# Optimization experiments

Hardware: AMD Instinct MI355X
Metric: run time of the kernel (lower is better)

Reference implementation:

```python
import jax, jax.numpy as jnp
import numpy as np

CHUNK = 256  # points per lax.map step; keeps [CHUNK, F] intermediates small


def _point_tri_sqdist(p_chunk, a, b, c):
    """Squared distance from each point to each triangle (Ericson closest-point).
    p_chunk: [C,3]; a,b,c: [F,3] -> returns [C,F]."""
    p = p_chunk[:, None, :]          # [C,1,3]
    a = a[None]; b = b[None]; c = c[None]  # [1,F,3]
    ab = b - a
    ac = c - a
    ap = p - a
    d1 = jnp.sum(ab * ap, -1)
    d2 = jnp.sum(ac * ap, -1)
    bp = p - b
    d3 = jnp.sum(ab * bp, -1)
    d4 = jnp.sum(ac * bp, -1)
    cp = p - c
    d5 = jnp.sum(ab * cp, -1)
    d6 = jnp.sum(ac * cp, -1)
    vc_ = d1 * d4 - d3 * d2
    vb_ = d5 * d2 - d1 * d6
    va_ = d3 * d6 - d5 * d4
    # safe-guarded edge / interior parameters
    den_ab = d1 - d3
    v_ab = d1 / jnp.where(den_ab != 0, den_ab, 1.0)
    den_ac = d2 - d6
    w_ac = d2 / jnp.where(den_ac != 0, den_ac, 1.0)
    den_bc = (d4 - d3) + (d5 - d6)
    w_bc = (d4 - d3) / jnp.where(den_bc != 0, den_bc, 1.0)
    den_in = va_ + vb_ + vc_
    inv = 1.0 / jnp.where(den_in != 0, den_in, 1.0)
    v_in = vb_ * inv
    w_in = vc_ * inv
    # candidate closest point; later writes take priority (vertex regions last)
    q = a + ab * v_in[..., None] + ac * w_in[..., None]                      # interior
    q = jnp.where(((va_ <= 0) & (d4 - d3 >= 0) & (d5 - d6 >= 0))[..., None],
                  b + (c - b) * w_bc[..., None], q)                          # edge bc
    q = jnp.where(((vb_ <= 0) & (d2 >= 0) & (d6 <= 0))[..., None],
                  a + ac * w_ac[..., None], q)                               # edge ac
    q = jnp.where(((vc_ <= 0) & (d1 >= 0) & (d3 <= 0))[..., None],
                  a + ab * v_ab[..., None], q)                               # edge ab
    q = jnp.where(((d6 >= 0) & (d5 <= d6))[..., None], c, q)                 # vertex c
    q = jnp.where(((d3 >= 0) & (d4 <= d3))[..., None], b, q)                 # vertex b
    q = jnp.where(((d1 <= 0) & (d2 <= 0))[..., None], a, q)                  # vertex a
    return jnp.sum((p - q) ** 2, -1)


def _mesh_sdf(verts, faces, points):
    va = verts[faces[:, 0]]
    vb = verts[faces[:, 1]]
    vc = verts[faces[:, 2]]

    def per_chunk(pc):
        d = _point_tri_sqdist(pc, va, vb, vc)   # [CHUNK, F]
        return jnp.min(d, axis=-1), jnp.argmin(d, axis=-1)

    P = points.shape[0]
    dists, assoc = jax.lax.map(per_chunk, points.reshape(P // CHUNK, CHUNK, 3))
    dist = dists.reshape(P)
    assoc = assoc.reshape(P).astype(jnp.int32)
    loss = jnp.sum(dist)
    return loss, dist, assoc


def setup_inputs() -> dict:
    key = jax.random.key(0)
    k1, k2, k3 = jax.random.split(key, 3)
    V, F, P = 8192, 16384, 16384
    verts = jax.random.uniform(k1, (V, 3), dtype=jnp.float32)
    faces = jax.random.randint(k2, (F, 3), 0, V, dtype=jnp.int32)
    points = jax.random.uniform(k3, (P, 3), dtype=jnp.float32)
    return {"verts": verts, "faces": faces, "points": points}


def reference(verts, faces, points):
    return _mesh_sdf(verts, faces, points)
```

## Files before the change

### kernel.cpp

```cpp
#include <hip/hip_runtime.h>
#include <math.h>


#define PTOT 16384
#define FTOT 16384
#define NBINS 4096
#define BLOCK 256
#define NCH 16
#define FCHUNK (FTOT / NCH)
#define TILE 256
#define QD 16

#define WS_BEST    0
#define WS_SORTP   131072
#define WS_HISTP   393216
#define WS_HISTF   409600
#define WS_HISTFC  425984
#define WS_FA      442368
#define WS_FB      704512
#define WS_FC      966656
#define WS_FSPH    1228800
#define WS_FSCAN   1490944
#define WS_FK      1753088

__device__ __forceinline__ unsigned morton12(float x, float y, float z) {
    int ix = (int)(x * 16.0f); ix = ix < 0 ? 0 : (ix > 15 ? 15 : ix);
    int iy = (int)(y * 16.0f); iy = iy < 0 ? 0 : (iy > 15 ? 15 : iy);
    int iz = (int)(z * 16.0f); iz = iz < 0 ? 0 : (iz > 15 ? 15 : iz);
    unsigned code = 0;
#pragma unroll
    for (int k = 0; k < 4; ++k) {
        code |= (((unsigned)(ix >> k) & 1u) << (3 * k + 2))
              | (((unsigned)(iy >> k) & 1u) << (3 * k + 1))
              | (((unsigned)(iz >> k) & 1u) << (3 * k + 0));
    }
    return code;
}

__device__ __forceinline__ float exec_pair(
    float px, float py, float pz,
    float ax, float ay, float az,
    float bx, float by, float bz,
    float cx, float cy, float cz)
{
#pragma clang fp contract(off)
    const float abx = __fsub_rn(bx, ax), aby = __fsub_rn(by, ay), abz = __fsub_rn(bz, az);
    const float acx = __fsub_rn(cx, ax), acy = __fsub_rn(cy, ay), acz = __fsub_rn(cz, az);
    const float cbx = __fsub_rn(cx, bx), cby = __fsub_rn(cy, by), cbz = __fsub_rn(cz, bz);

    const float apx = __fsub_rn(px, ax), apy = __fsub_rn(py, ay), apz = __fsub_rn(pz, az);
    const float d1 = __fadd_rn(__fadd_rn(__fmul_rn(abx, apx), __fmul_rn(aby, apy)), __fmul_rn(abz, apz));
    const float d2 = __fadd_rn(__fadd_rn(__fmul_rn(acx, apx), __fmul_rn(acy, apy)), __fmul_rn(acz, apz));
    const float bpx = __fsub_rn(px, bx), bpy = __fsub_rn(py, by), bpz = __fsub_rn(pz, bz);
    const float d3 = __fadd_rn(__fadd_rn(__fmul_rn(abx, bpx), __fmul_rn(aby, bpy)), __fmul_rn(abz, bpz));
    const float d4 = __fadd_rn(__fadd_rn(__fmul_rn(acx, bpx), __fmul_rn(acy, bpy)), __fmul_rn(acz, bpz));
    const float cpx = __fsub_rn(px, cx), cpy = __fsub_rn(py, cy), cpz = __fsub_rn(pz, cz);
    const float d5 = __fadd_rn(__fadd_rn(__fmul_rn(abx, cpx), __fmul_rn(aby, cpy)), __fmul_rn(abz, cpz));
    const float d6 = __fadd_rn(__fadd_rn(__fmul_rn(acx, cpx), __fmul_rn(acy, cpy)), __fmul_rn(acz, cpz));

    const float vc_ = __fsub_rn(__fmul_rn(d1, d4), __fmul_rn(d3, d2));
    const float vb_ = __fsub_rn(__fmul_rn(d5, d2), __fmul_rn(d1, d6));
    const float va_ = __fsub_rn(__fmul_rn(d3, d6), __fmul_rn(d5, d4));

    const float den_ab = __fsub_rn(d1, d3);
    const float den_ac = __fsub_rn(d2, d6);
    const float t43    = __fsub_rn(d4, d3);
    const float t56    = __fsub_rn(d5, d6);
    const float den_bc = __fadd_rn(t43, t56);
    const float den_in = __fadd_rn(__fadd_rn(va_, vb_), vc_);

    const bool f_a  = (d1 <= 0.0f) && (d2 <= 0.0f);
    const bool f_b  = (d3 >= 0.0f) && (d4 <= d3);
    const bool f_c  = (d6 >= 0.0f) && (d5 <= d6);
    const bool f_ab = (vc_ <= 0.0f) && (d1 >= 0.0f) && (d3 <= 0.0f);
    const bool f_ac = (vb_ <= 0.0f) && (d2 >= 0.0f) && (d6 <= 0.0f);
    const bool f_bc = (va_ <= 0.0f) && (t43 >= 0.0f) && (t56 >= 0.0f);
    const bool vert = f_a || f_b || f_c;
    const bool e_ab = f_ab && !vert;
    const bool e_ac = f_ac && !vert && !f_ab;
    const bool e_bc = f_bc && !vert && !f_ab && !f_ac;
    const bool inte = !vert && !f_ab && !f_ac && !f_bc;

    const float num  = e_ab ? d1 : (e_ac ? d2 : (e_bc ? t43 : 1.0f));
    const float denr = e_ab ? den_ab : (e_ac ? den_ac : (e_bc ? den_bc : den_in));
    const float den  = (denr != 0.0f) ? denr : 1.0f;
    const float t    = __fdiv_rn(num, den);

    const float v_in = __fmul_rn(vb_, t);
    const float w_in = __fmul_rn(vc_, t);

    const float s1 = vert ? 0.0f : (inte ? v_in : t);
    const float s2 = inte ? w_in : 0.0f;
    const bool  sel_b = (!f_a && f_b) || e_bc;
    const bool  sel_c = !f_a && !f_b && f_c;
    const float e1x = e_ac ? acx : (e_bc ? cbx : abx);
    const float e1y = e_ac ? acy : (e_bc ? cby : aby);
    const float e1z = e_ac ? acz : (e_bc ? cbz : abz);
    const float bsx = sel_b ? bx : (sel_c ? cx : ax);
    const float bsy = sel_b ? by : (sel_c ? cy : ay);
    const float bsz = sel_b ? bz : (sel_c ? cz : az);
    const float qx = __fadd_rn(__fadd_rn(bsx, __fmul_rn(e1x, s1)), __fmul_rn(acx, s2));
    const float qy = __fadd_rn(__fadd_rn(bsy, __fmul_rn(e1y, s1)), __fmul_rn(acy, s2));
    const float qz = __fadd_rn(__fadd_rn(bsz, __fmul_rn(e1z, s1)), __fmul_rn(acz, s2));

    const float dxx = __fsub_rn(px, qx), dyy = __fsub_rn(py, qy), dzz = __fsub_rn(pz, qz);
    return __fadd_rn(__fadd_rn(__fmul_rn(dxx, dxx), __fmul_rn(dyy, dyy)), __fmul_rn(dzz, dzz));
}

__global__ __launch_bounds__(BLOCK) void hist_kernel(
    const float* __restrict__ verts, const int* __restrict__ faces,
    const float* __restrict__ points,
    unsigned* __restrict__ histP, unsigned* __restrict__ histF)
{
    const int b = blockIdx.x;
    if (b < 64) {
        const int p = b * BLOCK + threadIdx.x;
        atomicAdd(&histP[morton12(points[p*3], points[p*3+1], points[p*3+2])], 1u);
    } else {
        const int f = (b - 64) * BLOCK + threadIdx.x;
        const int i0 = faces[f*3+0], i1 = faces[f*3+1], i2 = faces[f*3+2];
        const float mx = (verts[i0*3+0] + verts[i1*3+0] + verts[i2*3+0]) * (1.0f/3.0f);
        const float my = (verts[i0*3+1] + verts[i1*3+1] + verts[i2*3+1]) * (1.0f/3.0f);
        const float mz = (verts[i0*3+2] + verts[i1*3+2] + verts[i2*3+2]) * (1.0f/3.0f);
        atomicAdd(&histF[morton12(mx, my, mz)], 1u);
    }
}

__global__ __launch_bounds__(256) void scan_kernel(
    unsigned* __restrict__ histP, unsigned* __restrict__ histF,
    unsigned* __restrict__ histFC)
{
    unsigned* h = (blockIdx.x == 0) ? histP : histF;
    __shared__ unsigned ps[256];
    const int t = threadIdx.x;
    unsigned local[16];
    unsigned run = 0;
#pragma unroll
    for (int i = 0; i < 16; ++i) { unsigned v = h[t*16+i]; local[i] = run; run += v; }
    ps[t] = run;
    __syncthreads();
    for (int off = 1; off < 256; off <<= 1) {
        unsigned v = (t >= off) ? ps[t - off] : 0u;
        __syncthreads();
        ps[t] += v;
        __syncthreads();
    }
    const unsigned base = (t == 0) ? 0u : ps[t-1];
#pragma unroll
    for (int i = 0; i < 16; ++i) {
        const unsigned off = base + local[i];
        h[t*16+i] = off;
        if (blockIdx.x == 1) histFC[t*16+i] = off;
    }
}

__global__ __launch_bounds__(BLOCK) void scatter_build_kernel(
    const float* __restrict__ verts, const int* __restrict__ faces,
    const float* __restrict__ points,
    unsigned* __restrict__ histP, unsigned* __restrict__ histF,
    uint4* __restrict__ sortP,
    float4* __restrict__ fA, float4* __restrict__ fB, float4* __restrict__ fC,
    float4* __restrict__ fSph, float4* __restrict__ fScan,
    float2* __restrict__ fK)
{
    const int b = blockIdx.x;
    if (b < 64) {
        const int p = b * BLOCK + threadIdx.x;
        const float x = points[p*3], y = points[p*3+1], z = points[p*3+2];
        const unsigned pos = atomicAdd(&histP[morton12(x, y, z)], 1u);
        sortP[pos] = make_uint4(__float_as_uint(x), __float_as_uint(y),
                                __float_as_uint(z), (unsigned)p);
        return;
    }
    const int f = (b - 64) * BLOCK + threadIdx.x;
    const int i0 = faces[f*3+0], i1 = faces[f*3+1], i2 = faces[f*3+2];
    const float ax = verts[i0*3+0], ay = verts[i0*3+1], az = verts[i0*3+2];
    const float bx = verts[i1*3+0], by = verts[i1*3+1], bz = verts[i1*3+2];
    const float cx = verts[i2*3+0], cy = verts[i2*3+1], cz = verts[i2*3+2];
    const float mx = (ax+bx+cx) * (1.0f/3.0f);
    const float my = (ay+by+cy) * (1.0f/3.0f);
    const float mz = (az+bz+cz) * (1.0f/3.0f);
    const unsigned pos = atomicAdd(&histF[morton12(mx, my, mz)], 1u);

    fA[pos] = make_float4(ax, ay, az, __uint_as_float((unsigned)f));
    fB[pos] = make_float4(bx, by, bz, 0.0f);
    fC[pos] = make_float4(cx, cy, cz, 0.0f);

    const double abx = (double)bx-ax, aby = (double)by-ay, abz = (double)bz-az;
    const double acx = (double)cx-ax, acy = (double)cy-ay, acz = (double)cz-az;
    const double cbx = (double)cx-bx, cby = (double)cy-by, cbz = (double)cz-bz;
    const double nx = aby*acz - abz*acy;
    const double ny = abz*acx - abx*acz;
    const double nz = abx*acy - aby*acx;
    const double nn = nx*nx + ny*ny + nz*nz;
    const double e1 = sqrt(abx*abx + aby*aby + abz*abz);
    const double e2 = sqrt(acx*acx + acy*acy + acz*acz);
    const double e3 = sqrt(cbx*cbx + cby*cby + cbz*cbz);
    const double maxe = fmax(e1, fmax(e2, e3));
    const double mine = fmin(e1, fmin(e2, e3));
    const double mine2 = mine * mine;
    const double maxe2 = maxe * maxe;
    const double maxe3 = maxe2 * maxe;

    const bool exempt = !(nn > 1e-5 * maxe2) || !(mine2 > 5e-6 * maxe);

    float4 sc;
    float kp, J;
    if (!exempt) {
        const double rin = 1.0 / sqrt(nn);
        sc.x = (float)(nx * rin);
        sc.y = (float)(ny * rin);
        sc.z = (float)(nz * rin);
        sc.w = (float)(-(nx*rin*ax + ny*rin*ay + nz*rin*az));
        kp = (float)fmin(1e4, 3e-5 * maxe3 / nn + 2e-5);
        J  = (float)fmin(1e4, 1.2 * (6e-5 * maxe3 / nn
                                   + 5e-5 * maxe2 / mine2
                                   + 2.6e-6 * maxe / mine
                                   + 3.2e-3));
    } else {
        sc = make_float4(0.0f, 0.0f, 0.0f, 0.0f);
        kp = 1e4f;
        J  = 1e30f;
    }
    fScan[pos] = sc;
    fK[pos] = make_float2(kp, J);

    const double ra = sqrt(((double)ax-mx)*((double)ax-mx) + ((double)ay-my)*((double)ay-my) + ((double)az-mz)*((double)az-mz));
    const double rb = sqrt(((double)bx-mx)*((double)bx-mx) + ((double)by-my)*((double)by-my) + ((double)bz-mz)*((double)bz-mz));
    const double rc = sqrt(((double)cx-mx)*((double)cx-mx) + ((double)cy-my)*((double)cy-my) + ((double)cz-mz)*((double)cz-mz));
    const float rf = (float)(fmax(ra, fmax(rb, rc)) * 1.0002 + 2e-4);
    fSph[pos] = make_float4(mx, my, mz, rf);
}

__global__ __launch_bounds__(BLOCK) void sdf_main_kernel(
    const uint4* __restrict__ sortP,
    const unsigned* __restrict__ histFC,
    const float4* __restrict__ fA, const float4* __restrict__ fB,
    const float4* __restrict__ fC, const float4* __restrict__ fSph,
    const float4* __restrict__ fScan, const float2* __restrict__ fK,
    unsigned long long* __restrict__ best)
{
    __shared__ float4 sScan[TILE], sSph[TILE], sA[TILE], sB[TILE], sC[TILE];
    __shared__ float2 sK[TILE];
    __shared__ unsigned short sQ[TILE * QD];

    const int tid = threadIdx.x;
    const uint4 sp = sortP[blockIdx.x * BLOCK + tid];
    const float px = __uint_as_float(sp.x);
    const float py = __uint_as_float(sp.y);
    const float pz = __uint_as_float(sp.z);
    const int  pid = (int)sp.w;

    unsigned long long bestPk = ~0ull;
    {
        const unsigned code = morton12(px, py, pz);
        int w = (int)histFC[code] - 16;
        w = w < 0 ? 0 : (w > FTOT - 32 ? FTOT - 32 : w);
#pragma unroll
        for (int s = 0; s < 2; ++s) {
            const int i = w + 2 * (int)blockIdx.y + s;
            const float4 A = fA[i], B = fB[i], C = fC[i];
            const float d = exec_pair(px, py, pz, A.x, A.y, A.z, B.x, B.y, B.z, C.x, C.y, C.z);
            const unsigned long long pk =
                ((unsigned long long)__float_as_uint(d) << 32) | __float_as_uint(A.w);
            if (pk < bestPk) bestPk = pk;
        }
    }
    {
        const unsigned long long old = atomicMin(&best[pid], bestPk);
        if (old < bestPk) bestPk = old;
    }
    float pruneS = sqrtf(__uint_as_float((unsigned)(bestPk >> 32)));
    float thr    = __fmaf_rn(pruneS, 1.005f, 1e-3f);

    const int fbase = (int)blockIdx.y * FCHUNK;
    int cnt = 0;

    auto drain = [&]() {
        for (int k = 0; ; ++k) {
            if (!__ballot(k < cnt)) break;
            if (k < cnt) {
                const int j = (int)sQ[tid * QD + k];
                const float4 sc = sScan[j];
                const float4 S  = sSph[j];
                const float dx = px - S.x, dy = py - S.y, dz = pz - S.z;
                const float dcc2 = __fmaf_rn(dx, dx, __fmaf_rn(dy, dy, dz * dz));
                const float pdc  = __fmaf_rn(sc.x, dx, __fmaf_rn(sc.y, dy, sc.z * dz));
                const float pd   = __fmaf_rn(sc.x, px, __fmaf_rn(sc.y, py, __fmaf_rn(sc.z, pz, sc.w)));
                const float aa   = fmaxf(fabsf(pd) - 1e-5f, 0.0f);
                const float lat2 = fmaxf(dcc2 - pdc * pdc, 0.0f);
                const float lat  = fmaxf(sqrtf(lat2) * 0.999f - S.w - 1e-4f, 0.0f);
                const float lhs  = __fmaf_rn(aa, aa, lat * lat);
                const float rhs  = thr + sK[j].y;
                if (!(lhs > rhs * rhs)) {
                    const float4 A = sA[j], B = sB[j], C = sC[j];
                    const float d = exec_pair(px, py, pz, A.x, A.y, A.z, B.x, B.y, B.z, C.x, C.y, C.z);
                    const unsigned long long pk =
                        ((unsigned long long)__float_as_uint(d) << 32) | __float_as_uint(A.w);
                    if (pk < bestPk) {
                        bestPk = pk;
                        pruneS = fminf(pruneS, sqrtf(d));
                        thr    = __fmaf_rn(pruneS, 1.005f, 1e-3f);
                    }
                }
            }
        }
        cnt = 0;
    };

    for (int t0 = 0; t0 < FCHUNK; t0 += TILE) {
        __syncthreads();
        {
            const int g = fbase + t0 + tid;
            sScan[tid] = fScan[g];
            sSph[tid]  = fSph[g];
            sK[tid]    = fK[g];
            sA[tid]    = fA[g];
            sB[tid]    = fB[g];
            sC[tid]    = fC[g];
        }
        __syncthreads();

        {
            const unsigned long long gb =
                __hip_atomic_load(&best[pid], __ATOMIC_RELAXED, __HIP_MEMORY_SCOPE_AGENT);
            if (gb < bestPk) bestPk = gb;
            pruneS = fminf(pruneS, sqrtf(__uint_as_float((unsigned)(bestPk >> 32))));
            thr    = __fmaf_rn(pruneS, 1.005f, 1e-3f);
        }

        for (int j0 = 0; j0 < TILE; j0 += 8) {
#pragma unroll
            for (int j = j0; j < j0 + 8; ++j) {
                const float4 sc = sScan[j];
                const float pd = __fmaf_rn(sc.x, px, __fmaf_rn(sc.y, py, __fmaf_rn(sc.z, pz, sc.w)));
                const bool inband = !(fabsf(pd) > (thr + sK[j].x));
                if (inband) { sQ[tid * QD + cnt] = (unsigned short)j; ++cnt; }
            }
            if (__any(cnt >= QD - 8)) drain();
        }
        drain();
    }

    atomicMin(&best[pid], bestPk);
}

__global__ __launch_bounds__(BLOCK) void sdf_final_kernel(
    const unsigned long long* __restrict__ best, float* __restrict__ out)
{
    __shared__ float wsum[BLOCK / 64];
    const int p = blockIdx.x * BLOCK + threadIdx.x;
    const unsigned long long v = best[p];
    const float d = __uint_as_float((unsigned)(v >> 32));
    const int idx = (int)(unsigned)(v & 0xffffffffull);
    out[1 + p] = d;
    out[1 + PTOT + p] = (float)idx;

    float s = d;
    for (int off = 32; off > 0; off >>= 1) s += __shfl_down(s, off, 64);
    const int lane = threadIdx.x & 63;
    const int w = threadIdx.x >> 6;
    if (lane == 0) wsum[w] = s;
    __syncthreads();
    if (threadIdx.x == 0) {
        float tsum = 0.0f;
        for (int i = 0; i < BLOCK / 64; ++i) tsum += wsum[i];
        atomicAdd(&out[0], tsum);
    }
}

extern "C" void kernel_launch(void* const* d_in, const int* in_sizes, int n_in,
                              void* d_out, int out_size, void* d_ws, size_t ws_size,
                              hipStream_t stream) {
    const float* verts  = (const float*)d_in[0];
    const int*   faces  = (const int*)d_in[1];
    const float* points = (const float*)d_in[2];
    float* out = (float*)d_out;

    char* ws = (char*)d_ws;
    unsigned long long* best = (unsigned long long*)(ws + WS_BEST);
    uint4*    sortP  = (uint4*)(ws + WS_SORTP);
    unsigned* histP  = (unsigned*)(ws + WS_HISTP);
    unsigned* histF  = (unsigned*)(ws + WS_HISTF);
    unsigned* histFC = (unsigned*)(ws + WS_HISTFC);
    float4* fA    = (float4*)(ws + WS_FA);
    float4* fB    = (float4*)(ws + WS_FB);
    float4* fC    = (float4*)(ws + WS_FC);
    float4* fSph  = (float4*)(ws + WS_FSPH);
    float4* fScan = (float4*)(ws + WS_FSCAN);
    float2* fK    = (float2*)(ws + WS_FK);

    hipMemsetAsync(best, 0xFF, (size_t)PTOT * sizeof(unsigned long long), stream);
    hipMemsetAsync(histP, 0, 2 * (size_t)NBINS * sizeof(unsigned), stream);
    hipMemsetAsync(out, 0, sizeof(float), stream);

    hist_kernel<<<128, BLOCK, 0, stream>>>(verts, faces, points, histP, histF);
    scan_kernel<<<2, 256, 0, stream>>>(histP, histF, histFC);
    scatter_build_kernel<<<128, BLOCK, 0, stream>>>(verts, faces, points,
        histP, histF, sortP, fA, fB, fC, fSph, fScan, fK);

    dim3 grid(PTOT / BLOCK, NCH);
    sdf_main_kernel<<<grid, BLOCK, 0, stream>>>(sortP, histFC,
        fA, fB, fC, fSph, fScan, fK, best);
    sdf_final_kernel<<<PTOT / BLOCK, BLOCK, 0, stream>>>(best, out);
}
```

Measured before the change: 371.2 us.

## Double face-chunk split and read triangle vertices from global memory

Raises the number of face chunks per point block from 16 to 32, so the grid has twice as many blocks, each scanning half as many faces. Triangle vertex arrays are no longer staged in LDS. The exact distance test now reads A/B/C from global memory (L2/L1) only for faces that survive pruning, and the initial seed evaluates one nearby face instead of two. The intent is more parallelism and less LDS traffic and footprint, at the cost of more atomics, more redundant tile loads of the scan data, and scattered global reads. The old drain lambda is left behind as dead code.

```diff
diff --git a/kernel.cpp b/kernel.cpp
--- a/kernel.cpp
+++ b/kernel.cpp
@@ -6,7 +6,7 @@
 #define FTOT 16384
 #define NBINS 4096
 #define BLOCK 256
-#define NCH 16
+#define NCH 32
 #define FCHUNK (FTOT / NCH)
 #define TILE 256
 #define QD 16
@@ -240,7 +240,8 @@
     const float4* __restrict__ fScan, const float2* __restrict__ fK,
     unsigned long long* __restrict__ best)
 {
-    __shared__ float4 sScan[TILE], sSph[TILE], sA[TILE], sB[TILE], sC[TILE];
+    __shared__ float4 sScan[TILE];
+    __shared__ float4 sSph[TILE];
     __shared__ float2 sK[TILE];
     __shared__ unsigned short sQ[TILE * QD];
 
@@ -256,15 +257,10 @@
         const unsigned code = morton12(px, py, pz);
         int w = (int)histFC[code] - 16;
         w = w < 0 ? 0 : (w > FTOT - 32 ? FTOT - 32 : w);
-#pragma unroll
-        for (int s = 0; s < 2; ++s) {
-            const int i = w + 2 * (int)blockIdx.y + s;
-            const float4 A = fA[i], B = fB[i], C = fC[i];
-            const float d = exec_pair(px, py, pz, A.x, A.y, A.z, B.x, B.y, B.z, C.x, C.y, C.z);
-            const unsigned long long pk =
-                ((unsigned long long)__float_as_uint(d) << 32) | __float_as_uint(A.w);
-            if (pk < bestPk) bestPk = pk;
-        }
+        const int i = w + (int)blockIdx.y;
+        const float4 A = fA[i], B = fB[i], C = fC[i];
+        const float d = exec_pair(px, py, pz, A.x, A.y, A.z, B.x, B.y, B.z, C.x, C.y, C.z);
+        bestPk = ((unsigned long long)__float_as_uint(d) << 32) | __float_as_uint(A.w);
     }
     {
         const unsigned long long old = atomicMin(&best[pid], bestPk);
@@ -293,31 +289,25 @@
                 const float lhs  = __fmaf_rn(aa, aa, lat * lat);
                 const float rhs  = thr + sK[j].y;
                 if (!(lhs > rhs * rhs)) {
-                    const float4 A = sA[j], B = sB[j], C = sC[j];
-                    const float d = exec_pair(px, py, pz, A.x, A.y, A.z, B.x, B.y, B.z, C.x, C.y, C.z);
-                    const unsigned long long pk =
-                        ((unsigned long long)__float_as_uint(d) << 32) | __float_as_uint(A.w);
-                    if (pk < bestPk) {
-                        bestPk = pk;
-                        pruneS = fminf(pruneS, sqrtf(d));
-                        thr    = __fmaf_rn(pruneS, 1.005f, 1e-3f);
-                    }
+                    const int gi = fbase  + j;
+                    (void)gi;
+                    const int fi = (int)sQ[tid * QD + k] + 0;
+                    (void)fi;
                 }
             }
         }
         cnt = 0;
     };
+    (void)drain;
 
     for (int t0 = 0; t0 < FCHUNK; t0 += TILE) {
+        const int tileBase = fbase + t0;
         __syncthreads();
         {
-            const int g = fbase + t0 + tid;
+            const int g = tileBase + tid;
             sScan[tid] = fScan[g];
             sSph[tid]  = fSph[g];
             sK[tid]    = fK[g];
-            sA[tid]    = fA[g];
-            sB[tid]    = fB[g];
-            sC[tid]    = fC[g];
         }
         __syncthreads();
 
@@ -328,6 +318,40 @@
             pruneS = fminf(pruneS, sqrtf(__uint_as_float((unsigned)(bestPk >> 32))));
             thr    = __fmaf_rn(pruneS, 1.005f, 1e-3f);
         }
+
+        auto drainT = [&]() {
+            for (int k = 0; ; ++k) {
+                if (!__ballot(k < cnt)) break;
+                if (k < cnt) {
+                    const int j = (int)sQ[tid * QD + k];
+                    const float4 sc = sScan[j];
+                    const float4 S  = sSph[j];
+                    const float dx = px - S.x, dy = py - S.y, dz = pz - S.z;
+                    const float dcc2 = __fmaf_rn(dx, dx, __fmaf_rn(dy, dy, dz * dz));
+                    const float pdc  = __fmaf_rn(sc.x, dx, __fmaf_rn(sc.y, dy, sc.z * dz));
+                    const float pd   = __fmaf_rn(sc.x, px, __fmaf_rn(sc.y, py, __fmaf_rn(sc.z, pz, sc.w)));
+                    const float aa   = fmaxf(fabsf(pd) - 1e-5f, 0.0f);
+                    const float lat2 = fmaxf(dcc2 - pdc * pdc, 0.0f);
+                    const float lat  = fmaxf(sqrtf(lat2) * 0.999f - S.w - 1e-4f, 0.0f);
+                    const float lhs  = __fmaf_rn(aa, aa, lat * lat);
+                    const float rhs  = thr + sK[j].y;
+                    if (!(lhs > rhs * rhs)) {
+                        const int fi = tileBase + j;
+                        const float4 A = fA[fi], B = fB[fi], C = fC[fi];
+                        const float d = exec_pair(px, py, pz,
+                            A.x, A.y, A.z, B.x, B.y, B.z, C.x, C.y, C.z);
+                        const unsigned long long pk =
+                            ((unsigned long long)__float_as_uint(d) << 32) | __float_as_uint(A.w);
+                        if (pk < bestPk) {
+                            bestPk = pk;
+                            pruneS = fminf(pruneS, sqrtf(d));
+                            thr    = __fmaf_rn(pruneS, 1.005f, 1e-3f);
+                        }
+                    }
+                }
+            }
+            cnt = 0;
+        };
 
         for (int j0 = 0; j0 < TILE; j0 += 8) {
 #pragma unroll
@@ -337,9 +361,9 @@
                 const bool inband = !(fabsf(pd) > (thr + sK[j].x));
                 if (inband) { sQ[tid * QD + cnt] = (unsigned short)j; ++cnt; }
             }
-            if (__any(cnt >= QD - 8)) drain();
+            if (__any(cnt >= QD - 8)) drainT();
         }
-        drain();
+        drainT();
     }
 
     atomicMin(&best[pid], bestPk);
```

Result: no change. 366.7 us (-1.2%).

## Drop sphere/J secondary culling, use per-tile max slab width, split faces into 32 chunks

Applied to the files above, without the earlier changes.

The per-face bounding-sphere and J-bound secondary test is removed, and the per-face slab width is replaced by a per-256-face tile maximum built with atomicMax. Candidate triangle vertices are now read from global memory instead of shared memory, and shared usage drops to the plane array and the queue. The face dimension is split across 32 chunks instead of 16, the queue write becomes branchless with a transposed layout, and the best distance is published after each tile. This trades fewer shared loads and higher occupancy for weaker pruning, so more exact point-triangle evaluations run, and it adds a coarser tile-level bound.

```diff
diff --git a/kernel.cpp b/kernel.cpp
--- a/kernel.cpp
+++ b/kernel.cpp
@@ -6,7 +6,7 @@
 #define FTOT 16384
 #define NBINS 4096
 #define BLOCK 256
-#define NCH 16
+#define NCH 32
 #define FCHUNK (FTOT / NCH)
 #define TILE 256
 #define QD 16
@@ -15,13 +15,13 @@
 #define WS_SORTP   131072
 #define WS_HISTP   393216
 #define WS_HISTF   409600
-#define WS_HISTFC  425984
-#define WS_FA      442368
-#define WS_FB      704512
-#define WS_FC      966656
-#define WS_FSPH    1228800
-#define WS_FSCAN   1490944
-#define WS_FK      1753088
+#define WS_TILEKP  425984
+#define WS_HISTFC  426240
+#define WS_FA      442624
+#define WS_FB      704768
+#define WS_FC      966912
+#define WS_FSCAN   1229056
+#define ZERO_BYTES (16384 + 16384 + 256)
 
 __device__ __forceinline__ unsigned morton12(float x, float y, float z) {
     int ix = (int)(x * 16.0f); ix = ix < 0 ? 0 : (ix > 15 ? 15 : ix);
@@ -160,8 +160,7 @@
     unsigned* __restrict__ histP, unsigned* __restrict__ histF,
     uint4* __restrict__ sortP,
     float4* __restrict__ fA, float4* __restrict__ fB, float4* __restrict__ fC,
-    float4* __restrict__ fSph, float4* __restrict__ fScan,
-    float2* __restrict__ fK)
+    float4* __restrict__ fScan, unsigned* __restrict__ tileKp)
 {
     const int b = blockIdx.x;
     if (b < 64) {
@@ -198,51 +197,36 @@
     const double e3 = sqrt(cbx*cbx + cby*cby + cbz*cbz);
     const double maxe = fmax(e1, fmax(e2, e3));
     const double mine = fmin(e1, fmin(e2, e3));
-    const double mine2 = mine * mine;
     const double maxe2 = maxe * maxe;
     const double maxe3 = maxe2 * maxe;
 
-    const bool exempt = !(nn > 1e-5 * maxe2) || !(mine2 > 5e-6 * maxe);
+    const bool exempt = !(nn > 1e-5 * maxe2) || !(mine*mine > 5e-6 * maxe);
 
     float4 sc;
-    float kp, J;
     if (!exempt) {
         const double rin = 1.0 / sqrt(nn);
         sc.x = (float)(nx * rin);
         sc.y = (float)(ny * rin);
         sc.z = (float)(nz * rin);
         sc.w = (float)(-(nx*rin*ax + ny*rin*ay + nz*rin*az));
-        kp = (float)fmin(1e4, 3e-5 * maxe3 / nn + 2e-5);
-        J  = (float)fmin(1e4, 1.2 * (6e-5 * maxe3 / nn
-                                   + 5e-5 * maxe2 / mine2
-                                   + 2.6e-6 * maxe / mine
-                                   + 3.2e-3));
+        const float kp = (float)fmin(1e4, 3e-5 * maxe3 / nn + 2e-5);
+        atomicMax(&tileKp[pos >> 8], __float_as_uint(kp));
     } else {
         sc = make_float4(0.0f, 0.0f, 0.0f, 0.0f);
-        kp = 1e4f;
-        J  = 1e30f;
     }
     fScan[pos] = sc;
-    fK[pos] = make_float2(kp, J);
-
-    const double ra = sqrt(((double)ax-mx)*((double)ax-mx) + ((double)ay-my)*((double)ay-my) + ((double)az-mz)*((double)az-mz));
-    const double rb = sqrt(((double)bx-mx)*((double)bx-mx) + ((double)by-my)*((double)by-my) + ((double)bz-mz)*((double)bz-mz));
-    const double rc = sqrt(((double)cx-mx)*((double)cx-mx) + ((double)cy-my)*((double)cy-my) + ((double)cz-mz)*((double)cz-mz));
-    const float rf = (float)(fmax(ra, fmax(rb, rc)) * 1.0002 + 2e-4);
-    fSph[pos] = make_float4(mx, my, mz, rf);
 }
 
 __global__ __launch_bounds__(BLOCK) void sdf_main_kernel(
     const uint4* __restrict__ sortP,
     const unsigned* __restrict__ histFC,
     const float4* __restrict__ fA, const float4* __restrict__ fB,
-    const float4* __restrict__ fC, const float4* __restrict__ fSph,
-    const float4* __restrict__ fScan, const float2* __restrict__ fK,
+    const float4* __restrict__ fC, const float4* __restrict__ fScan,
+    const unsigned* __restrict__ tileKp,
     unsigned long long* __restrict__ best)
 {
-    __shared__ float4 sScan[TILE], sSph[TILE], sA[TILE], sB[TILE], sC[TILE];
-    __shared__ float2 sK[TILE];
-    __shared__ unsigned short sQ[TILE * QD];
+    __shared__ float4 sScan[TILE];
+    __shared__ unsigned short sQ[QD * BLOCK];
 
     const int tid = threadIdx.x;
     const uint4 sp = sortP[blockIdx.x * BLOCK + tid];
@@ -258,88 +242,66 @@
         w = w < 0 ? 0 : (w > FTOT - 32 ? FTOT - 32 : w);
 #pragma unroll
         for (int s = 0; s < 2; ++s) {
-            const int i = w + 2 * (int)blockIdx.y + s;
+            const int i = w + (int)((blockIdx.y + 16u * s) & 31u);
             const float4 A = fA[i], B = fB[i], C = fC[i];
             const float d = exec_pair(px, py, pz, A.x, A.y, A.z, B.x, B.y, B.z, C.x, C.y, C.z);
             const unsigned long long pk =
                 ((unsigned long long)__float_as_uint(d) << 32) | __float_as_uint(A.w);
             if (pk < bestPk) bestPk = pk;
         }
-    }
-    {
         const unsigned long long old = atomicMin(&best[pid], bestPk);
         if (old < bestPk) bestPk = old;
     }
-    float pruneS = sqrtf(__uint_as_float((unsigned)(bestPk >> 32)));
-    float thr    = __fmaf_rn(pruneS, 1.005f, 1e-3f);
 
     const int fbase = (int)blockIdx.y * FCHUNK;
     int cnt = 0;
 
-    auto drain = [&]() {
-        for (int k = 0; ; ++k) {
-            if (!__ballot(k < cnt)) break;
-            if (k < cnt) {
-                const int j = (int)sQ[tid * QD + k];
-                const float4 sc = sScan[j];
-                const float4 S  = sSph[j];
-                const float dx = px - S.x, dy = py - S.y, dz = pz - S.z;
-                const float dcc2 = __fmaf_rn(dx, dx, __fmaf_rn(dy, dy, dz * dz));
-                const float pdc  = __fmaf_rn(sc.x, dx, __fmaf_rn(sc.y, dy, sc.z * dz));
-                const float pd   = __fmaf_rn(sc.x, px, __fmaf_rn(sc.y, py, __fmaf_rn(sc.z, pz, sc.w)));
-                const float aa   = fmaxf(fabsf(pd) - 1e-5f, 0.0f);
-                const float lat2 = fmaxf(dcc2 - pdc * pdc, 0.0f);
-                const float lat  = fmaxf(sqrtf(lat2) * 0.999f - S.w - 1e-4f, 0.0f);
-                const float lhs  = __fmaf_rn(aa, aa, lat * lat);
-                const float rhs  = thr + sK[j].y;
-                if (!(lhs > rhs * rhs)) {
-                    const float4 A = sA[j], B = sB[j], C = sC[j];
-                    const float d = exec_pair(px, py, pz, A.x, A.y, A.z, B.x, B.y, B.z, C.x, C.y, C.z);
-                    const unsigned long long pk =
-                        ((unsigned long long)__float_as_uint(d) << 32) | __float_as_uint(A.w);
-                    if (pk < bestPk) {
-                        bestPk = pk;
-                        pruneS = fminf(pruneS, sqrtf(d));
-                        thr    = __fmaf_rn(pruneS, 1.005f, 1e-3f);
-                    }
-                }
-            }
-        }
-        cnt = 0;
-    };
-
     for (int t0 = 0; t0 < FCHUNK; t0 += TILE) {
+        const int tileBase = fbase + t0;
         __syncthreads();
-        {
-            const int g = fbase + t0 + tid;
-            sScan[tid] = fScan[g];
-            sSph[tid]  = fSph[g];
-            sK[tid]    = fK[g];
-            sA[tid]    = fA[g];
-            sB[tid]    = fB[g];
-            sC[tid]    = fC[g];
-        }
+        sScan[tid] = fScan[tileBase + tid];
         __syncthreads();
 
         {
             const unsigned long long gb =
                 __hip_atomic_load(&best[pid], __ATOMIC_RELAXED, __HIP_MEMORY_SCOPE_AGENT);
             if (gb < bestPk) bestPk = gb;
-            pruneS = fminf(pruneS, sqrtf(__uint_as_float((unsigned)(bestPk >> 32))));
-            thr    = __fmaf_rn(pruneS, 1.005f, 1e-3f);
         }
+        const float bestS = sqrtf(__uint_as_float((unsigned)(bestPk >> 32)));
+        const float thr   = __fmaf_rn(bestS, 1.005f, 1e-3f);
+        const float sThrL = thr + __uint_as_float(tileKp[tileBase >> 8]);
+
+        auto drainT = [&]() {
+            for (int k = 0; ; ++k) {
+                if (!__ballot(k < cnt)) break;
+                if (k < cnt) {
+                    const int fi = tileBase + (int)sQ[k * BLOCK + tid];
+                    const float4 A = fA[fi], B = fB[fi], C = fC[fi];
+                    const float d = exec_pair(px, py, pz,
+                        A.x, A.y, A.z, B.x, B.y, B.z, C.x, C.y, C.z);
+                    const unsigned long long pk =
+                        ((unsigned long long)__float_as_uint(d) << 32) | __float_as_uint(A.w);
+                    if (pk < bestPk) bestPk = pk;
+                }
+            }
+            cnt = 0;
+        };
 
         for (int j0 = 0; j0 < TILE; j0 += 8) {
 #pragma unroll
             for (int j = j0; j < j0 + 8; ++j) {
                 const float4 sc = sScan[j];
                 const float pd = __fmaf_rn(sc.x, px, __fmaf_rn(sc.y, py, __fmaf_rn(sc.z, pz, sc.w)));
-                const bool inband = !(fabsf(pd) > (thr + sK[j].x));
-                if (inband) { sQ[tid * QD + cnt] = (unsigned short)j; ++cnt; }
+                const int inband = (fabsf(pd) <= sThrL) ? 1 : 0;
+                sQ[cnt * BLOCK + tid] = (unsigned short)j;
+                cnt += inband;
             }
-            if (__any(cnt >= QD - 8)) drain();
+            if (__any(cnt >= QD - 8)) drainT();
         }
-        drain();
+        drainT();
+
+        const unsigned long long old = atomicMin(&best[pid], bestPk);
+        if (old < bestPk) bestPk = old;
     }
 
     atomicMin(&best[pid], bestPk);
@@ -382,25 +344,24 @@
     uint4*    sortP  = (uint4*)(ws + WS_SORTP);
     unsigned* histP  = (unsigned*)(ws + WS_HISTP);
     unsigned* histF  = (unsigned*)(ws + WS_HISTF);
+    unsigned* tileKp = (unsigned*)(ws + WS_TILEKP);
     unsigned* histFC = (unsigned*)(ws + WS_HISTFC);
     float4* fA    = (float4*)(ws + WS_FA);
     float4* fB    = (float4*)(ws + WS_FB);
     float4* fC    = (float4*)(ws + WS_FC);
-    float4* fSph  = (float4*)(ws + WS_FSPH);
     float4* fScan = (float4*)(ws + WS_FSCAN);
-    float2* fK    = (float2*)(ws + WS_FK);
 
     hipMemsetAsync(best, 0xFF, (size_t)PTOT * sizeof(unsigned long long), stream);
-    hipMemsetAsync(histP, 0, 2 * (size_t)NBINS * sizeof(unsigned), stream);
+    hipMemsetAsync(histP, 0, (size_t)ZERO_BYTES, stream);
     hipMemsetAsync(out, 0, sizeof(float), stream);
 
     hist_kernel<<<128, BLOCK, 0, stream>>>(verts, faces, points, histP, histF);
     scan_kernel<<<2, 256, 0, stream>>>(histP, histF, histFC);
     scatter_build_kernel<<<128, BLOCK, 0, stream>>>(verts, faces, points,
-        histP, histF, sortP, fA, fB, fC, fSph, fScan, fK);
+        histP, histF, sortP, fA, fB, fC, fScan, tileKp);
 
     dim3 grid(PTOT / BLOCK, NCH);
     sdf_main_kernel<<<grid, BLOCK, 0, stream>>>(sortP, histFC,
-        fA, fB, fC, fSph, fScan, fK, best);
+        fA, fB, fC, fScan, tileKp, best);
     sdf_final_kernel<<<PTOT / BLOCK, BLOCK, 0, stream>>>(best, out);
 }
```

Measured after the change: 684.6 us. 84.4% more time.
